# Kernel tuning notes

Hardware: AMD Instinct MI355X
Metric: run time of the kernel (lower is better)

The kernel has to match this reference:

```python
import jax, jax.numpy as jnp
import numpy as np
from jax import lax

NPOINT, NSAMPLE, RADIUS = 1024, 32, 0.2
IN_CH, DIM, HEADS = 64, 128, 4


def _fps(xyz, npoint):
    """Farthest point sampling. xyz: [B,N,3] -> idx [B,npoint] (int32)."""
    B, N, _ = xyz.shape

    def step(carry, _):
        dist, farthest = carry
        centroid = jnp.take_along_axis(xyz, farthest[:, None, None], axis=1)  # [B,1,3]
        d = jnp.sum((xyz - centroid) ** 2, axis=-1)                            # [B,N]
        dist = jnp.minimum(dist, d)
        nxt = jnp.argmax(dist, axis=-1).astype(jnp.int32)
        return (dist, nxt), farthest

    init = (jnp.full((B, N), 1e10, xyz.dtype), jnp.zeros((B,), jnp.int32))
    _, idxs = lax.scan(step, init, None, length=npoint)
    return idxs.T  # [B,npoint]


def _ball_query(radius, nsample, xyz, new_xyz):
    """xyz [B,N,3], new_xyz [B,S,3] -> idx [B,S,nsample]."""
    N = xyz.shape[1]
    sqr = jnp.sum((new_xyz[:, :, None, :] - xyz[:, None, :, :]) ** 2, axis=-1)  # [B,S,N]
    idx = jnp.broadcast_to(jnp.arange(N, dtype=jnp.int32), sqr.shape)
    idx = jnp.where(sqr > radius * radius, N, idx)
    idx = jnp.sort(idx, axis=-1)[..., :nsample]
    first = idx[..., :1]  # center itself always within radius -> valid
    return jnp.where(idx == N, first, idx)


_gather = jax.vmap(lambda a, i: a[i])  # a [N,C], i [S,K] -> [S,K,C]


def _forward(xyz, points, Wc, bc, gamma, beta, mean, var, Wq, Wk, Wv, Wo, Wp, bp):
    xyz_n = xyz.transpose(0, 2, 1)    # [B,N,3]
    pts = points.transpose(0, 2, 1)   # [B,N,D]

    fidx = _fps(xyz_n, NPOINT)                                         # [B,S]
    new_xyz = jnp.take_along_axis(xyz_n, fidx[:, :, None], axis=1)     # [B,S,3]
    gidx = _ball_query(RADIUS, NSAMPLE, xyz_n, new_xyz)                # [B,S,K]

    grouped_xyz = _gather(xyz_n, gidx)                                 # [B,S,K,3]
    rel = grouped_xyz - new_xyz[:, :, None, :]
    grouped_pts = _gather(pts, gidx)                                   # [B,S,K,D]
    feat = jnp.concatenate([rel, grouped_pts], axis=-1)                # [B,S,K,3+D]

    # 1x1 Conv2d + BatchNorm (inference form with running stats)
    h = jnp.einsum('bskc,dc->bskd', feat, Wc) + bc
    h = (h - mean) * gamma * lax.rsqrt(var + 1e-5) + beta              # [B,S,K,DIM]

    # local transformer: xyz positional encoding + MHSA over the K neighbors
    pos = jnp.einsum('bskc,cd->bskd', grouped_xyz, Wp) + bp
    x = h + pos
    B, S, K, D = x.shape
    hd = D // HEADS
    q = (x @ Wq).reshape(B, S, K, HEADS, hd)
    k = (x @ Wk).reshape(B, S, K, HEADS, hd)
    v = (x @ Wv).reshape(B, S, K, HEADS, hd)
    attn = jax.nn.softmax(jnp.einsum('bsqhd,bskhd->bshqk', q, k) * (hd ** -0.5), axis=-1)
    o = jnp.einsum('bshqk,bskhd->bsqhd', attn, v).reshape(B, S, K, D)
    out = x + o @ Wo                                                   # [B,S,K,DIM]

    new_points = jnp.max(out, axis=2).transpose(0, 2, 1)               # [B,DIM,S]
    return new_xyz.transpose(0, 2, 1), new_points


def setup_inputs() -> dict:
    key = jax.random.key(0)
    ks = jax.random.split(key, 9)
    C = IN_CH + 3
    s = lambda k, shp: (jax.random.normal(k, shp, jnp.float32) * 0.02)
    return dict(
        xyz=jax.random.uniform(ks[0], (8, 3, 4096), jnp.float32),
        points=jax.random.normal(ks[1], (8, IN_CH, 4096), jnp.float32),
        Wc=s(ks[2], (DIM, C)), bc=jnp.zeros((DIM,), jnp.float32),
        gamma=jnp.ones((DIM,), jnp.float32), beta=jnp.zeros((DIM,), jnp.float32),
        mean=jnp.zeros((DIM,), jnp.float32), var=jnp.ones((DIM,), jnp.float32),
        Wq=s(ks[3], (DIM, DIM)), Wk=s(ks[4], (DIM, DIM)),
        Wv=s(ks[5], (DIM, DIM)), Wo=s(ks[6], (DIM, DIM)),
        Wp=s(ks[7], (3, DIM)), bp=jnp.zeros((DIM,), jnp.float32),
    )


def reference(xyz, points, Wc, bc, gamma, beta, mean, var, Wq, Wk, Wv, Wo, Wp, bp):
    return _forward(xyz, points, Wc, bc, gamma, beta, mean, var, Wq, Wk, Wv, Wo, Wp, bp)
```

## Files before the change

### kernel.cpp

```cpp
#include <hip/hip_runtime.h>
#include <math.h>

#define B 8
#define N 4096
#define S 1024
#define K 32
#define CIN 64
#define DIM 128
#define NH 4
#define HD 32
#define PTROW 68

typedef __attribute__((ext_vector_type(8))) short bfrag;
typedef __attribute__((ext_vector_type(4))) float f32x4;

#define MFMA(a, b, c) __builtin_amdgcn_mfma_f32_16x16x32_bf16((a), (b), (c), 0, 0, 0)

__device__ __forceinline__ unsigned short f2bf(float f) {
    union { float f; unsigned u; } v; v.f = f;
    unsigned r = v.u + 0x7FFFu + ((v.u >> 16) & 1u);
    return (unsigned short)(r >> 16);
}

__global__ void k_prep(const float* __restrict__ Wc, const float* __restrict__ bc,
                       const float* __restrict__ gamma, const float* __restrict__ beta,
                       const float* __restrict__ mean, const float* __restrict__ var,
                       const float* __restrict__ Wp, const float* __restrict__ bp,
                       float* __restrict__ Wall) {
    int d = threadIdx.x;
    if (d >= DIM) return;
    float a = gamma[d] / sqrtf(var[d] + 1e-5f);
    for (int c = 0; c < 67; c++) Wall[c * DIM + d] = Wc[d * 67 + c] * a;
    for (int c = 0; c < 3; c++)  Wall[(67 + c) * DIM + d] = Wp[c * DIM + d];
    Wall[70 * DIM + d] = bc[d] * a + beta[d] - mean[d] * a + bp[d];
}

__global__ void k_prep2(const float* __restrict__ Wall, const float* __restrict__ Wq,
                        const float* __restrict__ Wk, const float* __restrict__ Wv,
                        const float* __restrict__ Wo, unsigned short* __restrict__ WF) {
    int blk = blockIdx.x;
    int mat, kt, base;
    if (blk < 3) { mat = 0; kt = blk; base = 0; }
    else { mat = 1 + (blk - 3) / 4; kt = (blk - 3) % 4; base = 12288 + (mat - 1) * 16384; }
    const float* W = (mat == 0) ? Wall : (mat == 1) ? Wq : (mat == 2) ? Wk : (mat == 3) ? Wv : Wo;
    int tid = threadIdx.x;
    int gnt = tid >> 6, lane = tid & 63;
    int n = gnt * 16 + (lane & 15);
    int k0 = kt * 32 + (lane >> 4) * 8;
    unsigned short* dst = WF + base + (size_t)((kt * 8 + gnt) * 64 + lane) * 8;
#pragma unroll
    for (int i = 0; i < 8; i++) {
        int k = k0 + i;
        float v = (mat == 0 && k >= 70) ? 0.0f : W[k * 128 + n];
        dst[i] = f2bf(v);
    }
}

__global__ void k_transpose(const float* __restrict__ xyz, const float* __restrict__ points,
                            float* __restrict__ ptsT) {
    int idx = blockIdx.x * 256 + threadIdx.x;
    const int total = B * N * PTROW;
    if (idx >= total) return;
    int c = idx % PTROW;
    int n = (idx / PTROW) % N;
    int b = idx / (PTROW * N);
    float v = 0.0f;
    if (c < 3) v = xyz[(b * 3 + c) * N + n];
    else if (c < 67) v = points[(b * CIN + (c - 3)) * N + n];
    ptsT[idx] = v;
}

#define FPS_DPP_STEP(CTRL) {                                                                       \
    unsigned h2 = (unsigned)__builtin_amdgcn_update_dpp((int)kh, (int)kh, CTRL, 0xf, 0xf, false);  \
    unsigned l2 = (unsigned)__builtin_amdgcn_update_dpp((int)kl, (int)kl, CTRL, 0xf, 0xf, false);  \
    unsigned long long curk = ((unsigned long long)kh << 32) | kl;                                 \
    unsigned long long nxtk = ((unsigned long long)h2 << 32) | l2;                                 \
    if (nxtk > curk) { kh = h2; kl = l2; }                                                         \
}

__global__ __launch_bounds__(256) void k_fps(const float* __restrict__ xyz,
                                             float* __restrict__ nxyz,
                                             float* __restrict__ out_xyz) {
    const int b = blockIdx.x;
    const float* X = xyz + (size_t)b * 3 * N;
    __shared__ float xs[N], ys[N], zs[N];
    __shared__ float cent[S * 3];
    __shared__ unsigned long long wbuf[2][4];
    const int tid = threadIdx.x;
    const int PT = N / 256;

    float px[16], py[16], pz[16], pd[16];
#pragma unroll
    for (int i = 0; i < PT; i++) {
        int n = tid + i * 256;
        px[i] = X[n]; py[i] = X[N + n]; pz[i] = X[2 * N + n];
        xs[n] = px[i]; ys[n] = py[i]; zs[n] = pz[i];
        pd[i] = 1e10f;
    }
    __syncthreads();

    float cx = xs[0], cy = ys[0], cz = zs[0];
    for (int t = 0; t < S; t++) {
        if (tid == 0) { cent[t * 3] = cx; cent[t * 3 + 1] = cy; cent[t * 3 + 2] = cz; }
        if (t == S - 1) break;

        float bv = -1.0f; int bi = 0;
#pragma unroll
        for (int i = 0; i < PT; i++) {
            float dx = px[i] - cx, dy = py[i] - cy, dz = pz[i] - cz;
            float d = __fadd_rn(__fadd_rn(__fmul_rn(dx, dx), __fmul_rn(dy, dy)), __fmul_rn(dz, dz));
            pd[i] = fminf(pd[i], d);
            if (pd[i] > bv) { bv = pd[i]; bi = tid + i * 256; }
        }
        unsigned kh = __float_as_uint(bv);
        unsigned kl = 0xFFFFFFFFu - (unsigned)bi;
        FPS_DPP_STEP(0x111)
        FPS_DPP_STEP(0x112)
        FPS_DPP_STEP(0x114)
        FPS_DPP_STEP(0x118)
        FPS_DPP_STEP(0x142)
        FPS_DPP_STEP(0x143)
        if ((tid & 63) == 63)
            wbuf[t & 1][tid >> 6] = ((unsigned long long)kh << 32) | kl;
        __syncthreads();
        unsigned long long k0 = wbuf[t & 1][0], k1 = wbuf[t & 1][1];
        unsigned long long k2 = wbuf[t & 1][2], k3 = wbuf[t & 1][3];
        unsigned long long kA = k0 > k1 ? k0 : k1;
        unsigned long long kB = k2 > k3 ? k2 : k3;
        unsigned long long km = kA > kB ? kA : kB;
        int best = (int)(0xFFFFFFFFu - (unsigned)km);
        cx = xs[best]; cy = ys[best]; cz = zs[best];
    }
    __syncthreads();
    for (int i = tid; i < S; i += 256) {
        float a = cent[i * 3], c1 = cent[i * 3 + 1], c2 = cent[i * 3 + 2];
        nxyz[(b * S + i) * 3 + 0] = a;
        nxyz[(b * S + i) * 3 + 1] = c1;
        nxyz[(b * S + i) * 3 + 2] = c2;
        out_xyz[b * 3 * S + i] = a;
        out_xyz[b * 3 * S + S + i] = c1;
        out_xyz[b * 3 * S + 2 * S + i] = c2;
    }
}

__global__ void k_ball(const float* __restrict__ xyz, const float* __restrict__ nxyz,
                       int* __restrict__ gidx) {
    const int g = blockIdx.x * 4 + (threadIdx.x >> 6);
    const int lane = threadIdx.x & 63;
    const int b = g >> 10;
    const float* X = xyz + (size_t)b * 3 * N;
    float cx = nxyz[g * 3 + 0], cy = nxyz[g * 3 + 1], cz = nxyz[g * 3 + 2];
    int cnt = 0;
    int first = -1;
    for (int base = 0; base < N && cnt < K; base += 64) {
        int n = base + lane;
        float dx = cx - X[n], dy = cy - X[N + n], dz = cz - X[2 * N + n];
        float d = __fadd_rn(__fadd_rn(__fmul_rn(dx, dx), __fmul_rn(dy, dy)), __fmul_rn(dz, dz));
        bool in = (d <= 0.04f);
        unsigned long long m = __ballot(in);
        int pre = __popcll(m & ((1ull << lane) - 1ull));
        if (in && cnt + pre < K) gidx[g * K + cnt + pre] = n;
        if (first < 0 && m) first = base + (int)__ffsll((unsigned long long)m) - 1;
        cnt += __popcll(m);
    }
    if (cnt < K) {
        for (int i = cnt + lane; i < K; i += 64) gidx[g * K + i] = first;
    }
}

#define LDS_X   0
#define LDS_A   8192
#define LDS_K   16384
#define LDS_VT  24576
#define LDS_MISC 38912
#define LDS_TOTAL 39056

#define LDSA_READ(off, row, colb) \
    (*(const bfrag*)(smem + (off) + ((row) << 8) + ((colb) ^ (((row) & 7) << 4))))
#define LDS_ST16(off, row, colb, val) \
    (*(unsigned short*)(smem + (off) + ((row) << 8) + ((colb) ^ (((row) & 7) << 4))) = (val))

__global__ __launch_bounds__(256, 4) void k_group(
    const float* __restrict__ ptsT, const float* __restrict__ nxyz,
    const int* __restrict__ gidx, const unsigned short* __restrict__ WF,
    const float* __restrict__ bias, float* __restrict__ outp) {
    __shared__ __align__(16) char smem[LDS_TOTAL];
    const int g = blockIdx.x, b = g >> 10, s = g & 1023;
    const int tid = threadIdx.x;
    const int w = tid >> 6, l = tid & 63;
    const int lane16 = l & 15, lquad = l >> 4;
    const int ncol = w * 32;

    int* nidx = (int*)(smem + LDS_MISC);
    float* ctr = (float*)(smem + LDS_MISC + 128);

    if (tid < K) nidx[tid] = gidx[g * K + tid];
    if (tid >= 64 && tid < 67) ctr[tid - 64] = nxyz[g * 3 + (tid - 64)];
    for (int i = tid; i < 32 * 32; i += 256) {
        int p = i >> 5, c = 64 + (i & 31);
        LDS_ST16(LDS_A, p, c * 2, (unsigned short)0);
    }
    __syncthreads();

    {
        const int p = tid >> 3, j = tid & 7;
        const float* src = ptsT + (size_t)(b * N + nidx[p]) * PTROW;
        float c0 = ctr[0], c1 = ctr[1], c2 = ctr[2];
        for (int c = j; c < 70; c += 8) {
            float v;
            if (c < 3) v = src[c] - (c == 0 ? c0 : c == 1 ? c1 : c2);
            else if (c < 67) v = src[c];
            else v = src[c - 67];
            LDS_ST16(LDS_A, p, c * 2, f2bf(v));
        }
    }
    __syncthreads();

    f32x4 accx[2][2];
    {
        float bv0 = bias[ncol + lane16], bv1 = bias[ncol + 16 + lane16];
        accx[0][0] = f32x4{bv0, bv0, bv0, bv0}; accx[1][0] = accx[0][0];
        accx[0][1] = f32x4{bv1, bv1, bv1, bv1}; accx[1][1] = accx[0][1];
        const bfrag* WallF = (const bfrag*)WF;
#pragma unroll
        for (int kt = 0; kt < 3; kt++) {
            bfrag a0 = LDSA_READ(LDS_A, lane16, kt * 64 + lquad * 16);
            bfrag a1 = LDSA_READ(LDS_A, 16 + lane16, kt * 64 + lquad * 16);
            bfrag b0 = WallF[(kt * 8 + w * 2 + 0) * 64 + l];
            bfrag b1 = WallF[(kt * 8 + w * 2 + 1) * 64 + l];
            accx[0][0] = MFMA(a0, b0, accx[0][0]);
            accx[0][1] = MFMA(a0, b1, accx[0][1]);
            accx[1][0] = MFMA(a1, b0, accx[1][0]);
            accx[1][1] = MFMA(a1, b1, accx[1][1]);
        }
#pragma unroll
        for (int mt = 0; mt < 2; mt++)
#pragma unroll
            for (int nt = 0; nt < 2; nt++)
#pragma unroll
                for (int r = 0; r < 4; r++)
                    LDS_ST16(LDS_X, mt * 16 + lquad * 4 + r, (ncol + nt * 16 + lane16) * 2,
                             f2bf(accx[mt][nt][r]));
    }
    __syncthreads();

    {
        const bfrag* WQF = (const bfrag*)(WF + 12288);
        const bfrag* WKF = (const bfrag*)(WF + 28672);
        const bfrag* WVF = (const bfrag*)(WF + 45056);
#pragma unroll
        for (int m = 0; m < 3; m++) {
            const bfrag* BW = (m == 0) ? WQF : (m == 1) ? WKF : WVF;
            f32x4 acc[2][2] = {};
#pragma unroll
            for (int kt = 0; kt < 4; kt++) {
                bfrag a0 = LDSA_READ(LDS_X, lane16, kt * 64 + lquad * 16);
                bfrag a1 = LDSA_READ(LDS_X, 16 + lane16, kt * 64 + lquad * 16);
                bfrag b0 = BW[(kt * 8 + w * 2 + 0) * 64 + l];
                bfrag b1 = BW[(kt * 8 + w * 2 + 1) * 64 + l];
                acc[0][0] = MFMA(a0, b0, acc[0][0]);
                acc[0][1] = MFMA(a0, b1, acc[0][1]);
                acc[1][0] = MFMA(a1, b0, acc[1][0]);
                acc[1][1] = MFMA(a1, b1, acc[1][1]);
            }
            if (m < 2) {
                int dst = (m == 0) ? LDS_A : LDS_K;
#pragma unroll
                for (int mt = 0; mt < 2; mt++)
#pragma unroll
                    for (int nt = 0; nt < 2; nt++)
#pragma unroll
                        for (int r = 0; r < 4; r++)
                            LDS_ST16(dst, mt * 16 + lquad * 4 + r, (ncol + nt * 16 + lane16) * 2,
                                     f2bf(acc[mt][nt][r]));
            } else {
#pragma unroll
                for (int mt = 0; mt < 2; mt++)
#pragma unroll
                    for (int nt = 0; nt < 2; nt++)
#pragma unroll
                        for (int r = 0; r < 4; r++) {
                            int d = ncol + nt * 16 + lane16;
                            int j = mt * 16 + lquad * 4 + r;
                            *(unsigned short*)(smem + LDS_VT + d * 112 + j * 2) = f2bf(acc[mt][nt][r]);
                        }
            }
        }
    }
    __syncthreads();

    {
        const int h = w;
        const int hb = h * 64;
        bfrag aq0 = LDSA_READ(LDS_A, lane16, hb + lquad * 16);
        bfrag aq1 = LDSA_READ(LDS_A, 16 + lane16, hb + lquad * 16);
        bfrag bk0 = LDSA_READ(LDS_K, lane16, hb + lquad * 16);
        bfrag bk1 = LDSA_READ(LDS_K, 16 + lane16, hb + lquad * 16);
        f32x4 sc[2][2] = {};
        sc[0][0] = MFMA(aq0, bk0, sc[0][0]);
        sc[0][1] = MFMA(aq0, bk1, sc[0][1]);
        sc[1][0] = MFMA(aq1, bk0, sc[1][0]);
        sc[1][1] = MFMA(aq1, bk1, sc[1][1]);

        const float scale = 0.17677669529663687f;
        float p_[2][2][4];
        float mx[2][4], sm[2][4];
#pragma unroll
        for (int mt = 0; mt < 2; mt++)
#pragma unroll
            for (int r = 0; r < 4; r++) {
                p_[mt][0][r] = sc[mt][0][r] * scale;
                p_[mt][1][r] = sc[mt][1][r] * scale;
                mx[mt][r] = fmaxf(p_[mt][0][r], p_[mt][1][r]);
            }
#pragma unroll
        for (int d = 1; d < 16; d <<= 1)
#pragma unroll
            for (int mt = 0; mt < 2; mt++)
#pragma unroll
                for (int r = 0; r < 4; r++)
                    mx[mt][r] = fmaxf(mx[mt][r], __shfl_xor(mx[mt][r], d));
#pragma unroll
        for (int mt = 0; mt < 2; mt++)
#pragma unroll
            for (int r = 0; r < 4; r++) {
                float e0 = __expf(p_[mt][0][r] - mx[mt][r]);
                float e1 = __expf(p_[mt][1][r] - mx[mt][r]);
                p_[mt][0][r] = e0; p_[mt][1][r] = e1;
                sm[mt][r] = e0 + e1;
            }
#pragma unroll
        for (int d = 1; d < 16; d <<= 1)
#pragma unroll
            for (int mt = 0; mt < 2; mt++)
#pragma unroll
                for (int r = 0; r < 4; r++)
                    sm[mt][r] += __shfl_xor(sm[mt][r], d);
#pragma unroll
        for (int mt = 0; mt < 2; mt++)
#pragma unroll
            for (int r = 0; r < 4; r++) {
                float inv = 1.0f / sm[mt][r];
                int row = mt * 16 + lquad * 4 + r;
                LDS_ST16(LDS_X, row, (h * 32 + lane16) * 2, f2bf(p_[mt][0][r] * inv));
                LDS_ST16(LDS_X, row, (h * 32 + 16 + lane16) * 2, f2bf(p_[mt][1][r] * inv));
            }

        f32x4 oacc[2][2] = {};
        bfrag ap0 = LDSA_READ(LDS_X, lane16, hb + lquad * 16);
        bfrag ap1 = LDSA_READ(LDS_X, 16 + lane16, hb + lquad * 16);
        bfrag bv0 = *(const bfrag*)(smem + LDS_VT + (h * 32 + lane16) * 112 + lquad * 16);
        bfrag bv1 = *(const bfrag*)(smem + LDS_VT + (h * 32 + 16 + lane16) * 112 + lquad * 16);
        oacc[0][0] = MFMA(ap0, bv0, oacc[0][0]);
        oacc[0][1] = MFMA(ap0, bv1, oacc[0][1]);
        oacc[1][0] = MFMA(ap1, bv0, oacc[1][0]);
        oacc[1][1] = MFMA(ap1, bv1, oacc[1][1]);
#pragma unroll
        for (int mt = 0; mt < 2; mt++)
#pragma unroll
            for (int nt = 0; nt < 2; nt++)
#pragma unroll
                for (int r = 0; r < 4; r++)
                    LDS_ST16(LDS_A, mt * 16 + lquad * 4 + r, (h * 32 + nt * 16 + lane16) * 2,
                             f2bf(oacc[mt][nt][r]));
    }
    __syncthreads();

    {
        const bfrag* WOF = (const bfrag*)(WF + 61440);
        f32x4 acc[2][2];
#pragma unroll
        for (int mt = 0; mt < 2; mt++)
#pragma unroll
            for (int nt = 0; nt < 2; nt++) acc[mt][nt] = accx[mt][nt];
#pragma unroll
        for (int kt = 0; kt < 4; kt++) {
            bfrag a0 = LDSA_READ(LDS_A, lane16, kt * 64 + lquad * 16);
            bfrag a1 = LDSA_READ(LDS_A, 16 + lane16, kt * 64 + lquad * 16);
            bfrag b0 = WOF[(kt * 8 + w * 2 + 0) * 64 + l];
            bfrag b1 = WOF[(kt * 8 + w * 2 + 1) * 64 + l];
            acc[0][0] = MFMA(a0, b0, acc[0][0]);
            acc[0][1] = MFMA(a0, b1, acc[0][1]);
            acc[1][0] = MFMA(a1, b0, acc[1][0]);
            acc[1][1] = MFMA(a1, b1, acc[1][1]);
        }
        float mnt[2];
#pragma unroll
        for (int nt = 0; nt < 2; nt++) {
            float m = acc[0][nt][0];
#pragma unroll
            for (int r = 1; r < 4; r++) m = fmaxf(m, acc[0][nt][r]);
#pragma unroll
            for (int r = 0; r < 4; r++) m = fmaxf(m, acc[1][nt][r]);
            m = fmaxf(m, __shfl_xor(m, 16));
            m = fmaxf(m, __shfl_xor(m, 32));
            mnt[nt] = m;
        }
        if (lquad == 0) {
#pragma unroll
            for (int nt = 0; nt < 2; nt++) {
                int d = ncol + nt * 16 + lane16;
                outp[((size_t)b * DIM + d) * S + s] = mnt[nt];
            }
        }
    }
}

extern "C" void kernel_launch(void* const* d_in, const int* in_sizes, int n_in,
                              void* d_out, int out_size, void* d_ws, size_t ws_size,
                              hipStream_t stream) {
    const float* xyz = (const float*)d_in[0];
    const float* points = (const float*)d_in[1];
    const float* Wc = (const float*)d_in[2];
    const float* bc = (const float*)d_in[3];
    const float* gamma = (const float*)d_in[4];
    const float* beta = (const float*)d_in[5];
    const float* mean = (const float*)d_in[6];
    const float* var = (const float*)d_in[7];
    const float* Wq = (const float*)d_in[8];
    const float* Wk = (const float*)d_in[9];
    const float* Wv = (const float*)d_in[10];
    const float* Wo = (const float*)d_in[11];
    const float* Wp = (const float*)d_in[12];
    const float* bp = (const float*)d_in[13];

    float* out_xyz = (float*)d_out;
    float* out_pts = out_xyz + B * 3 * S;

    char* ws = (char*)d_ws;
    float* ptsT = (float*)ws;
    size_t off = (size_t)B * N * PTROW * 4;
    float* nxyz = (float*)(ws + off); off += (size_t)B * S * 3 * 4;
    int* gidxp = (int*)(ws + off); off += (size_t)B * S * K * 4;
    float* Wall = (float*)(ws + off); off += 71 * DIM * 4;
    unsigned short* WF = (unsigned short*)(ws + off); off += 77824 * 2;

    k_prep<<<1, 128, 0, stream>>>(Wc, bc, gamma, beta, mean, var, Wp, bp, Wall);
    k_prep2<<<19, 512, 0, stream>>>(Wall, Wq, Wk, Wv, Wo, WF);
    k_transpose<<<(B * N * PTROW + 255) / 256, 256, 0, stream>>>(xyz, points, ptsT);
    k_fps<<<B, 256, 0, stream>>>(xyz, nxyz, out_xyz);
    k_ball<<<B * S / 4, 256, 0, stream>>>(xyz, nxyz, gidxp);
    k_group<<<B * S, 256, 0, stream>>>(ptsT, nxyz, gidxp, WF, Wall + 70 * DIM, out_pts);
}
```

Measured before the change: 750.8 us.

## Merge FPS, transpose and weight prep into one concurrent mega-kernel

Combines the weight preparation kernels, the point transpose and farthest point sampling into a single launch, where blocks are assigned different roles so the transpose and prep run alongside the serial FPS blocks. The FPS argmax reduction changes from a 64-bit key DPP reduction to a float max followed by a min-index reduction, and coordinates are stored interleaved in shared memory. The aim is to hide the transpose and prep work behind the long single-block-per-batch FPS and to cut launch overhead and per-step reduction cost. The shared-memory footprint applies to every block, including the transpose blocks, which may limit their occupancy.

Result: slower. 772.0 us (+2.8%).

```diff
diff --git a/kernel.cpp b/kernel.cpp
--- a/kernel.cpp
+++ b/kernel.cpp
@@ -10,6 +10,7 @@
 #define NH 4
 #define HD 32
 #define PTROW 68
+#define NT_BLOCKS 256
 
 typedef __attribute__((ext_vector_type(8))) short bfrag;
 typedef __attribute__((ext_vector_type(4))) float f32x4;
@@ -22,124 +23,148 @@
     return (unsigned short)(r >> 16);
 }
 
-__global__ void k_prep(const float* __restrict__ Wc, const float* __restrict__ bc,
-                       const float* __restrict__ gamma, const float* __restrict__ beta,
-                       const float* __restrict__ mean, const float* __restrict__ var,
-                       const float* __restrict__ Wp, const float* __restrict__ bp,
-                       float* __restrict__ Wall) {
-    int d = threadIdx.x;
-    if (d >= DIM) return;
-    float a = gamma[d] / sqrtf(var[d] + 1e-5f);
-    for (int c = 0; c < 67; c++) Wall[c * DIM + d] = Wc[d * 67 + c] * a;
-    for (int c = 0; c < 3; c++)  Wall[(67 + c) * DIM + d] = Wp[c * DIM + d];
-    Wall[70 * DIM + d] = bc[d] * a + beta[d] - mean[d] * a + bp[d];
-}
-
-__global__ void k_prep2(const float* __restrict__ Wall, const float* __restrict__ Wq,
-                        const float* __restrict__ Wk, const float* __restrict__ Wv,
-                        const float* __restrict__ Wo, unsigned short* __restrict__ WF) {
+#define DPPMAXF(var, CTRL) {                                                              \
+    int _o = __builtin_amdgcn_update_dpp(__float_as_int(var), __float_as_int(var),        \
+                                         CTRL, 0xf, 0xf, false);                          \
+    var = fmaxf(var, __int_as_float(_o));                                                 \
+}
+#define DPPMINU(var, CTRL) {                                                              \
+    unsigned _o = (unsigned)__builtin_amdgcn_update_dpp((int)(var), (int)(var),           \
+                                                        CTRL, 0xf, 0xf, false);          \
+    var = (_o < (var)) ? _o : (var);                                                      \
+}
+
+__global__ __launch_bounds__(256) void k_mega(
+    const float* __restrict__ xyz, const float* __restrict__ points,
+    const float* __restrict__ Wc, const float* __restrict__ bc,
+    const float* __restrict__ gamma, const float* __restrict__ beta,
+    const float* __restrict__ mean, const float* __restrict__ var,
+    const float* __restrict__ Wp, const float* __restrict__ bp,
+    const float* __restrict__ Wq, const float* __restrict__ Wk,
+    const float* __restrict__ Wv, const float* __restrict__ Wo,
+    float* __restrict__ ptsT, float* __restrict__ nxyz, float* __restrict__ out_xyz,
+    unsigned short* __restrict__ WF, float* __restrict__ biasv) {
+    __shared__ float pxyz[N * 3];
+    __shared__ float cent[S * 3];
+    __shared__ __align__(16) unsigned long long wbuf[2][4];
+    const int tid = threadIdx.x;
     int blk = blockIdx.x;
-    int mat, kt, base;
-    if (blk < 3) { mat = 0; kt = blk; base = 0; }
-    else { mat = 1 + (blk - 3) / 4; kt = (blk - 3) % 4; base = 12288 + (mat - 1) * 16384; }
-    const float* W = (mat == 0) ? Wall : (mat == 1) ? Wq : (mat == 2) ? Wk : (mat == 3) ? Wv : Wo;
-    int tid = threadIdx.x;
-    int gnt = tid >> 6, lane = tid & 63;
-    int n = gnt * 16 + (lane & 15);
-    int k0 = kt * 32 + (lane >> 4) * 8;
-    unsigned short* dst = WF + base + (size_t)((kt * 8 + gnt) * 64 + lane) * 8;
-#pragma unroll
-    for (int i = 0; i < 8; i++) {
-        int k = k0 + i;
-        float v = (mat == 0 && k >= 70) ? 0.0f : W[k * 128 + n];
-        dst[i] = f2bf(v);
-    }
-}
-
-__global__ void k_transpose(const float* __restrict__ xyz, const float* __restrict__ points,
-                            float* __restrict__ ptsT) {
-    int idx = blockIdx.x * 256 + threadIdx.x;
-    const int total = B * N * PTROW;
-    if (idx >= total) return;
-    int c = idx % PTROW;
-    int n = (idx / PTROW) % N;
-    int b = idx / (PTROW * N);
-    float v = 0.0f;
-    if (c < 3) v = xyz[(b * 3 + c) * N + n];
-    else if (c < 67) v = points[(b * CIN + (c - 3)) * N + n];
-    ptsT[idx] = v;
-}
-
-#define FPS_DPP_STEP(CTRL) {                                                                       \
-    unsigned h2 = (unsigned)__builtin_amdgcn_update_dpp((int)kh, (int)kh, CTRL, 0xf, 0xf, false);  \
-    unsigned l2 = (unsigned)__builtin_amdgcn_update_dpp((int)kl, (int)kl, CTRL, 0xf, 0xf, false);  \
-    unsigned long long curk = ((unsigned long long)kh << 32) | kl;                                 \
-    unsigned long long nxtk = ((unsigned long long)h2 << 32) | l2;                                 \
-    if (nxtk > curk) { kh = h2; kl = l2; }                                                         \
-}
-
-__global__ __launch_bounds__(256) void k_fps(const float* __restrict__ xyz,
-                                             float* __restrict__ nxyz,
-                                             float* __restrict__ out_xyz) {
-    const int b = blockIdx.x;
-    const float* X = xyz + (size_t)b * 3 * N;
-    __shared__ float xs[N], ys[N], zs[N];
-    __shared__ float cent[S * 3];
-    __shared__ unsigned long long wbuf[2][4];
-    const int tid = threadIdx.x;
-    const int PT = N / 256;
-
-    float px[16], py[16], pz[16], pd[16];
-#pragma unroll
-    for (int i = 0; i < PT; i++) {
-        int n = tid + i * 256;
-        px[i] = X[n]; py[i] = X[N + n]; pz[i] = X[2 * N + n];
-        xs[n] = px[i]; ys[n] = py[i]; zs[n] = pz[i];
-        pd[i] = 1e10f;
-    }
-    __syncthreads();
-
-    float cx = xs[0], cy = ys[0], cz = zs[0];
-    for (int t = 0; t < S; t++) {
-        if (tid == 0) { cent[t * 3] = cx; cent[t * 3 + 1] = cy; cent[t * 3 + 2] = cz; }
-        if (t == S - 1) break;
-
-        float bv = -1.0f; int bi = 0;
-#pragma unroll
-        for (int i = 0; i < PT; i++) {
-            float dx = px[i] - cx, dy = py[i] - cy, dz = pz[i] - cz;
-            float d = __fadd_rn(__fadd_rn(__fmul_rn(dx, dx), __fmul_rn(dy, dy)), __fmul_rn(dz, dz));
-            pd[i] = fminf(pd[i], d);
-            if (pd[i] > bv) { bv = pd[i]; bi = tid + i * 256; }
-        }
-        unsigned kh = __float_as_uint(bv);
-        unsigned kl = 0xFFFFFFFFu - (unsigned)bi;
-        FPS_DPP_STEP(0x111)
-        FPS_DPP_STEP(0x112)
-        FPS_DPP_STEP(0x114)
-        FPS_DPP_STEP(0x118)
-        FPS_DPP_STEP(0x142)
-        FPS_DPP_STEP(0x143)
-        if ((tid & 63) == 63)
-            wbuf[t & 1][tid >> 6] = ((unsigned long long)kh << 32) | kl;
+
+    if (blk < 8) {
+        const int b = blk;
+        const float* X = xyz + (size_t)b * 3 * N;
+        float px[16], py[16], pz[16], pd[16];
+#pragma unroll
+        for (int i = 0; i < 16; i++) {
+            int n = tid + i * 256;
+            px[i] = X[n]; py[i] = X[N + n]; pz[i] = X[2 * N + n];
+            pxyz[n * 3 + 0] = px[i];
+            pxyz[n * 3 + 1] = py[i];
+            pxyz[n * 3 + 2] = pz[i];
+            pd[i] = 1e10f;
+        }
         __syncthreads();
-        unsigned long long k0 = wbuf[t & 1][0], k1 = wbuf[t & 1][1];
-        unsigned long long k2 = wbuf[t & 1][2], k3 = wbuf[t & 1][3];
-        unsigned long long kA = k0 > k1 ? k0 : k1;
-        unsigned long long kB = k2 > k3 ? k2 : k3;
-        unsigned long long km = kA > kB ? kA : kB;
-        int best = (int)(0xFFFFFFFFu - (unsigned)km);
-        cx = xs[best]; cy = ys[best]; cz = zs[best];
-    }
-    __syncthreads();
-    for (int i = tid; i < S; i += 256) {
-        float a = cent[i * 3], c1 = cent[i * 3 + 1], c2 = cent[i * 3 + 2];
-        nxyz[(b * S + i) * 3 + 0] = a;
-        nxyz[(b * S + i) * 3 + 1] = c1;
-        nxyz[(b * S + i) * 3 + 2] = c2;
-        out_xyz[b * 3 * S + i] = a;
-        out_xyz[b * 3 * S + S + i] = c1;
-        out_xyz[b * 3 * S + 2 * S + i] = c2;
+        float cx = pxyz[0], cy = pxyz[1], cz = pxyz[2];
+
+        for (int t = 0; t < S; t++) {
+            if (tid == 0) { cent[t * 3] = cx; cent[t * 3 + 1] = cy; cent[t * 3 + 2] = cz; }
+            if (t == S - 1) break;
+
+            float bv = -1.0f; int slot = 0;
+#pragma unroll
+            for (int i = 0; i < 16; i++) {
+                float dx = px[i] - cx, dy = py[i] - cy, dz = pz[i] - cz;
+                float d = __fadd_rn(__fadd_rn(__fmul_rn(dx, dx), __fmul_rn(dy, dy)), __fmul_rn(dz, dz));
+                float pn = fminf(pd[i], d);
+                pd[i] = pn;
+                bool gt = pn > bv;
+                bv = gt ? pn : bv;
+                slot = gt ? i : slot;
+            }
+            float m = bv;
+            DPPMAXF(m, 0x111)
+            DPPMAXF(m, 0x112)
+            DPPMAXF(m, 0x114)
+            DPPMAXF(m, 0x118)
+            DPPMAXF(m, 0x142)
+            DPPMAXF(m, 0x143)
+            float wmax = __int_as_float(__builtin_amdgcn_readlane(__float_as_int(m), 63));
+            unsigned bi = (unsigned)(tid + (slot << 8));
+            unsigned bic = (bv == wmax) ? bi : 0xFFFFFFFFu;
+            DPPMINU(bic, 0x111)
+            DPPMINU(bic, 0x112)
+            DPPMINU(bic, 0x114)
+            DPPMINU(bic, 0x118)
+            DPPMINU(bic, 0x142)
+            DPPMINU(bic, 0x143)
+            if ((tid & 63) == 63) {
+                unsigned long long key =
+                    ((unsigned long long)__float_as_uint(wmax) << 32) | (0xFFFFFFFFu - bic);
+                wbuf[t & 1][tid >> 6] = key;
+            }
+            __syncthreads();
+            ulonglong2 ab = *(const ulonglong2*)&wbuf[t & 1][0];
+            ulonglong2 cd = *(const ulonglong2*)&wbuf[t & 1][2];
+            unsigned long long kA = ab.x > ab.y ? ab.x : ab.y;
+            unsigned long long kB = cd.x > cd.y ? cd.x : cd.y;
+            unsigned long long km = kA > kB ? kA : kB;
+            int best = (int)(0xFFFFFFFFu - (unsigned)km);
+            cx = pxyz[best * 3]; cy = pxyz[best * 3 + 1]; cz = pxyz[best * 3 + 2];
+        }
+        __syncthreads();
+        for (int i = tid; i < S; i += 256) {
+            float a = cent[i * 3], c1 = cent[i * 3 + 1], c2 = cent[i * 3 + 2];
+            nxyz[(b * S + i) * 3 + 0] = a;
+            nxyz[(b * S + i) * 3 + 1] = c1;
+            nxyz[(b * S + i) * 3 + 2] = c2;
+            out_xyz[b * 3 * S + i] = a;
+            out_xyz[b * 3 * S + S + i] = c1;
+            out_xyz[b * 3 * S + 2 * S + i] = c2;
+        }
+        return;
+    }
+    blk -= 8;
+    if (blk < NT_BLOCKS) {
+        const int total = B * N * PTROW;
+        for (int idx = blk * 256 + tid; idx < total; idx += NT_BLOCKS * 256) {
+            int c = idx % PTROW;
+            int n = (idx / PTROW) % N;
+            int b = idx / (PTROW * N);
+            float v = 0.0f;
+            if (c < 3) v = xyz[(b * 3 + c) * N + n];
+            else if (c < 67) v = points[(b * CIN + (c - 3)) * N + n];
+            ptsT[idx] = v;
+        }
+        return;
+    }
+    blk -= NT_BLOCKS;
+    if (blk < 19) {
+        int mat, kt, base;
+        if (blk < 3) { mat = 0; kt = blk; base = 0; }
+        else { mat = 1 + (blk - 3) / 4; kt = (blk - 3) % 4; base = 12288 + (mat - 1) * 16384; }
+        const float* W = (mat == 1) ? Wq : (mat == 2) ? Wk : (mat == 3) ? Wv : Wo;
+        const int lane = tid & 63;
+#pragma unroll
+        for (int g2 = 0; g2 < 2; g2++) {
+            int gnt = (tid >> 6) * 2 + g2;
+            int n = gnt * 16 + (lane & 15);
+            int k0 = kt * 32 + (lane >> 4) * 8;
+            unsigned short* dst = WF + base + (size_t)((kt * 8 + gnt) * 64 + lane) * 8;
+            float a = (mat == 0) ? (gamma[n] / sqrtf(var[n] + 1e-5f)) : 0.0f;
+#pragma unroll
+            for (int i = 0; i < 8; i++) {
+                int k = k0 + i;
+                float v;
+                if (mat == 0) v = (k < 67) ? Wc[n * 67 + k] * a : (k < 70) ? Wp[(k - 67) * 128 + n] : 0.0f;
+                else v = W[k * 128 + n];
+                dst[i] = f2bf(v);
+            }
+        }
+        return;
+    }
+    if (tid < DIM) {
+        float a = gamma[tid] / sqrtf(var[tid] + 1e-5f);
+        biasv[tid] = bc[tid] * a + beta[tid] - mean[tid] * a + bp[tid];
     }
 }
 
@@ -432,13 +457,12 @@
     size_t off = (size_t)B * N * PTROW * 4;
     float* nxyz = (float*)(ws + off); off += (size_t)B * S * 3 * 4;
     int* gidxp = (int*)(ws + off); off += (size_t)B * S * K * 4;
-    float* Wall = (float*)(ws + off); off += 71 * DIM * 4;
     unsigned short* WF = (unsigned short*)(ws + off); off += 77824 * 2;
-
-    k_prep<<<1, 128, 0, stream>>>(Wc, bc, gamma, beta, mean, var, Wp, bp, Wall);
-    k_prep2<<<19, 512, 0, stream>>>(Wall, Wq, Wk, Wv, Wo, WF);
-    k_transpose<<<(B * N * PTROW + 255) / 256, 256, 0, stream>>>(xyz, points, ptsT);
-    k_fps<<<B, 256, 0, stream>>>(xyz, nxyz, out_xyz);
+    float* biasv = (float*)(ws + off); off += DIM * 4;
+
+    k_mega<<<8 + NT_BLOCKS + 19 + 1, 256, 0, stream>>>(
+        xyz, points, Wc, bc, gamma, beta, mean, var, Wp, bp, Wq, Wk, Wv, Wo,
+        ptsT, nxyz, out_xyz, WF, biasv);
     k_ball<<<B * S / 4, 256, 0, stream>>>(xyz, nxyz, gidxp);
-    k_group<<<B * S, 256, 0, stream>>>(ptsT, nxyz, gidxp, WF, Wall + 70 * DIM, out_pts);
-}
+    k_group<<<B * S, 256, 0, stream>>>(ptsT, nxyz, gidxp, WF, biasv, out_pts);
+}
```
